# Kernel optimization log

Hardware: AMD Instinct MI355X
Metric: run time of the kernel (lower is better)

Reference implementation:

```python
import math
import jax, jax.numpy as jnp
import numpy as np

B, N, C_IN, C_OUT = 16, 1024, 256, 256


def setup_inputs() -> dict:
    key = jax.random.key(0)
    k_x, k_q, k_k, k_v, k_s, k_e = jax.random.split(key, 6)
    x = jax.random.normal(k_x, (B, N, C_IN), dtype=jnp.float32)
    # torch Linear(in, out, bias=False) == x @ W with W: [in, out]
    sc = 1.0 / math.sqrt(C_IN)
    W_q = jax.random.normal(k_q, (C_IN, C_OUT), dtype=jnp.float32) * sc
    W_k = jax.random.normal(k_k, (C_IN, C_OUT), dtype=jnp.float32) * sc
    W_v = jax.random.normal(k_v, (C_IN, C_OUT), dtype=jnp.float32) * sc
    W_sigma = jax.random.normal(k_s, (C_IN, 1), dtype=jnp.float32) * sc
    # fixed standard-normal noise replacing torch.normal's on-the-fly sampling
    eps = jax.random.normal(k_e, (B, N, N), dtype=jnp.float32)
    return {"x": x, "W_q": W_q, "W_k": W_k, "W_v": W_v,
            "W_sigma": W_sigma, "eps": eps}


def reference(x, W_q, W_k, W_v, W_sigma, eps):
    n = x.shape[1]
    d_model = W_q.shape[1]
    Q = x @ W_q            # [B, n, d]
    K = x @ W_k            # [B, n, d]
    V = x @ W_v            # [B, n, d]
    sigma = x @ W_sigma    # [B, n, 1]

    # prior association: gaussian = Normal(mean=|i-j|, std=|sigma|), row-normalized
    idx = jnp.arange(n)
    p = jnp.abs(idx[:, None] - idx[None, :]).astype(x.dtype)   # [n, n]
    gaussian = p[None, :, :] + jnp.abs(sigma) * eps            # [B, n, n]
    P = gaussian / jnp.sum(gaussian, axis=-1, keepdims=True)

    # series association: softmax over dim=0 (batch), exactly as the torch code
    scores = jnp.einsum('bnd,bmd->bnm', Q, K) / math.sqrt(d_model)
    S = jax.nn.softmax(scores, axis=0)

    Z = jnp.einsum('bnm,bmd->bnd', S, V)                       # reconstruction
    return Z, P, S
```

## Files before the change

kernel.cpp:

```cpp
#include <hip/hip_runtime.h>
#include <hip/hip_bf16.h>
#include <math.h>

#define B_ 16
#define N_ 1024
#define C_ 256

typedef unsigned short ushort_t;
typedef __attribute__((ext_vector_type(8))) short short8;
typedef __attribute__((ext_vector_type(4))) float f32x4;

static __device__ __forceinline__ ushort_t f2bf(float f) {
    __hip_bfloat16 h = __float2bfloat16(f);
    return *(ushort_t*)&h;
}

static __device__ __forceinline__ float bf2f(ushort_t u) {
    return __uint_as_float(((unsigned int)u) << 16);
}

static __device__ __forceinline__ void async16(const ushort_t* g, ushort_t* l) {
    __builtin_amdgcn_global_load_lds(
        (const __attribute__((address_space(1))) unsigned int*)g,
        (__attribute__((address_space(3))) unsigned int*)l,
        16, 0, 0);
}

template <int OUT_BF16, int SWZ>
__global__ __launch_bounds__(512) void gemm_nt_bf16(
    const ushort_t* __restrict__ A, const ushort_t* __restrict__ B,
    void* __restrict__ Cp, int M, int N, int K,
    long sA, long sB, long sC, float alpha)
{
    int bx = blockIdx.x, by = blockIdx.y, bz = blockIdx.z;
    if constexpr (SWZ) {
        const int gx = gridDim.x, gy = gridDim.y;
        const int nwg = gx * gy * (int)gridDim.z;
        const int lid = bx + gx * (by + gy * bz);
        const int cpx = nwg >> 3;
        const int s = (lid & 7) * cpx + (lid >> 3);
        bx = s % gx;
        const int t = s / gx;
        by = t % gy;
        bz = t / gy;
    }
    A += (long)bz * sA;
    B += (long)bz * sB;

    __shared__ ushort_t sh[2][2 * 128 * 32];
    float* shF = (float*)sh;

    const int tid  = threadIdx.x;
    const int wave = tid >> 6;
    const int lane = tid & 63;
    const int wm   = wave >> 2;
    const int wn   = wave & 3;
    const int row0 = by * 128;
    const int col0 = bx * 128;

    const int r_grp = lane >> 2;
    const int c_chk = lane & 3;
    const int swz   = c_chk ^ ((r_grp >> 1) & 3);

    const ushort_t* agp = A + (long)(row0 + wave * 16 + r_grp) * K + swz * 8;
    const ushort_t* bgp = B + (long)(col0 + wave * 16 + r_grp) * K + swz * 8;

    const int lr16 = lane & 15;
    const int q16  = lane >> 4;
    const int slot = (q16 ^ ((lr16 >> 1) & 3)) * 8;

    f32x4 acc[4][2] = {};

    {
        ushort_t* As = sh[0];
        ushort_t* Bs = sh[0] + 128 * 32;
        async16(agp, &As[wave * 512]);
        async16(bgp, &Bs[wave * 512]);
    }
    __syncthreads();

    int p = 0;
    for (int k0 = 0; k0 < K; k0 += 32) {
        if (k0 + 32 < K) {
            ushort_t* As = sh[p ^ 1];
            ushort_t* Bs = sh[p ^ 1] + 128 * 32;
            async16(agp + k0 + 32, &As[wave * 512]);
            async16(bgp + k0 + 32, &Bs[wave * 512]);
        }

        const ushort_t* As = sh[p];
        const ushort_t* Bs = sh[p] + 128 * 32;
        short8 av[4], bv[2];
#pragma unroll
        for (int i = 0; i < 4; i++)
            av[i] = *(const short8*)&As[(wm * 64 + i * 16 + lr16) * 32 + slot];
#pragma unroll
        for (int j = 0; j < 2; j++)
            bv[j] = *(const short8*)&Bs[(wn * 32 + j * 16 + lr16) * 32 + slot];

#pragma unroll
        for (int i = 0; i < 4; i++)
#pragma unroll
            for (int j = 0; j < 2; j++)
                acc[i][j] = __builtin_amdgcn_mfma_f32_16x16x32_bf16(
                    av[i], bv[j], acc[i][j], 0, 0, 0);

        __syncthreads();
        p ^= 1;
    }

#pragma unroll
    for (int i = 0; i < 4; i++) {
#pragma unroll
        for (int j = 0; j < 2; j++) {
            const int rl = wm * 16 + q16 * 4;
            const int cl = wn * 32 + j * 16 + lr16;
#pragma unroll
            for (int r = 0; r < 4; r++) {
                const int rr = rl + r;
                const int xr = ((rr >> 2) & 1) << 4;
                shF[rr * 128 + (cl ^ xr)] = alpha * acc[i][j][r];
            }
        }
        __syncthreads();

        if constexpr (OUT_BF16) {
            ushort_t* C = (ushort_t*)Cp + (long)bz * sC;
            const int idx = tid;
            const int rl = idx >> 4;
            const int c8 = idx & 15;
            const int xr4 = ((rl >> 2) & 1) << 2;
            const int gr = row0 + (rl >> 4) * 64 + i * 16 + (rl & 15);
            const float4 a = ((const float4*)(shF + rl * 128))[(c8 * 2) ^ xr4];
            const float4 b = ((const float4*)(shF + rl * 128))[(c8 * 2 + 1) ^ xr4];
            short8 pk;
            pk[0] = (short)f2bf(a.x); pk[1] = (short)f2bf(a.y);
            pk[2] = (short)f2bf(a.z); pk[3] = (short)f2bf(a.w);
            pk[4] = (short)f2bf(b.x); pk[5] = (short)f2bf(b.y);
            pk[6] = (short)f2bf(b.z); pk[7] = (short)f2bf(b.w);
            *(short8*)(C + (long)gr * N + col0 + c8 * 8) = pk;
        } else {
            float* C = (float*)Cp + (long)bz * sC;
#pragma unroll
            for (int v = 0; v < 2; v++) {
                const int idx = v * 512 + tid;
                const int rl = idx >> 5;
                const int c4 = idx & 31;
                const int xr4 = ((rl >> 2) & 1) << 2;
                const int gr = row0 + (rl >> 4) * 64 + i * 16 + (rl & 15);
                const float4 val = ((const float4*)(shF + rl * 128))[c4 ^ xr4];
                *(float4*)(C + (long)gr * N + col0 + c4 * 4) = val;
            }
        }
        __syncthreads();
    }
}

__global__ __launch_bounds__(256) void cast_fused(
    const float* __restrict__ x, ushort_t* __restrict__ xbf,
    const float* __restrict__ Wq, const float* __restrict__ Wk,
    const float* __restrict__ Wv, ushort_t* __restrict__ WbfT,
    const float* __restrict__ Wsig, float* __restrict__ asig)
{
    __shared__ float t[32][33];
    const int blk = blockIdx.x;
    if (blk < 4096) {
        const long i = ((long)blk * 256 + threadIdx.x) * 4;
        const float4 v = *(const float4*)(x + i);
        ushort4 o;
        o.x = f2bf(v.x); o.y = f2bf(v.y); o.z = f2bf(v.z); o.w = f2bf(v.w);
        *(ushort4*)(xbf + i) = o;
        if (asig) {
            const int lane = threadIdx.x & 63;
            const float4 w = *(const float4*)(Wsig + lane * 4);
            float d = v.x * w.x + v.y * w.y + v.z * w.z + v.w * w.w;
#pragma unroll
            for (int off = 32; off; off >>= 1) d += __shfl_down(d, off, 64);
            if (lane == 0) asig[blk * 4 + (threadIdx.x >> 6)] = fabsf(d);
        }
    } else {
        const int m = blk - 4096;
        const float* W = ((m >> 6) == 0) ? Wq : ((m >> 6) == 1) ? Wk : Wv;
        const int rem = m & 63;
        const int n0 = (rem & 7) * 32, k0 = (rem >> 3) * 32;
        const int tx = threadIdx.x & 31, ty = threadIdx.x >> 5;
#pragma unroll
        for (int j = 0; j < 4; j++)
            t[ty + j * 8][tx] = W[(long)(k0 + ty + j * 8) * 256 + n0 + tx];
        __syncthreads();
        ushort_t* o = WbfT + (long)(m >> 6) * 65536;
#pragma unroll
        for (int j = 0; j < 4; j++)
            o[(long)(n0 + ty + j * 8) * 256 + k0 + tx] = f2bf(t[tx][ty + j * 8]);
    }
}

__global__ __launch_bounds__(256) void transpose_v_kernel(
    const ushort_t* __restrict__ V, ushort_t* __restrict__ VT)
{
    __shared__ ushort_t t[32][33];
    const long NC = (long)N_ * C_;
    const ushort_t* Vb = V + (long)blockIdx.z * NC;
    ushort_t* Tb = VT + (long)blockIdx.z * NC;
    const int n0 = blockIdx.x * 32, m0 = blockIdx.y * 32;
    const int tx = threadIdx.x & 31, ty = threadIdx.x >> 5;
#pragma unroll
    for (int j = 0; j < 4; j++)
        t[ty + j * 8][tx] = Vb[(long)(m0 + ty + j * 8) * C_ + n0 + tx];
    __syncthreads();
#pragma unroll
    for (int j = 0; j < 4; j++)
        Tb[(long)(n0 + ty + j * 8) * N_ + m0 + tx] = t[tx][ty + j * 8];
}

__global__ __launch_bounds__(256) void softmax_batch(
    ushort_t* __restrict__ Sc, float* __restrict__ S)
{
    const long NN = (long)N_ * N_;
    const long i4 = ((long)blockIdx.x * 256 + threadIdx.x) * 4;

    float4 v[B_];
    float mx = -INFINITY, my = -INFINITY, mz = -INFINITY, mw = -INFINITY;
#pragma unroll
    for (int b = 0; b < B_; b++) {
        const ushort4 u = *(const ushort4*)(Sc + (long)b * NN + i4);
        v[b].x = bf2f(u.x); v[b].y = bf2f(u.y);
        v[b].z = bf2f(u.z); v[b].w = bf2f(u.w);
        mx = fmaxf(mx, v[b].x); my = fmaxf(my, v[b].y);
        mz = fmaxf(mz, v[b].z); mw = fmaxf(mw, v[b].w);
    }
    float sx = 0.f, sy = 0.f, sz = 0.f, sw = 0.f;
#pragma unroll
    for (int b = 0; b < B_; b++) {
        v[b].x = __expf(v[b].x - mx); sx += v[b].x;
        v[b].y = __expf(v[b].y - my); sy += v[b].y;
        v[b].z = __expf(v[b].z - mz); sz += v[b].z;
        v[b].w = __expf(v[b].w - mw); sw += v[b].w;
    }
    const float ix = 1.0f / sx, iy = 1.0f / sy, iz = 1.0f / sz, iw = 1.0f / sw;
#pragma unroll
    for (int b = 0; b < B_; b++) {
        float4 o;
        o.x = v[b].x * ix; o.y = v[b].y * iy;
        o.z = v[b].z * iz; o.w = v[b].w * iw;
        *(float4*)(S + (long)b * NN + i4) = o;
        ushort4 ob;
        ob.x = f2bf(o.x); ob.y = f2bf(o.y); ob.z = f2bf(o.z); ob.w = f2bf(o.w);
        *(ushort4*)(Sc + (long)b * NN + i4) = ob;
    }
}

__global__ __launch_bounds__(256) void p_kernel(
    const float* __restrict__ x, const float* __restrict__ Wsig,
    const float* __restrict__ eps, float* __restrict__ P,
    const float* __restrict__ asig)
{
    const int row  = blockIdx.x * 4 + (threadIdx.x >> 6);
    const int lane = threadIdx.x & 63;
    const int n = row & (N_ - 1);

    float a;
    if (asig) {
        a = asig[row];
    } else {
        const float4 xv = *(const float4*)(x + (long)row * C_ + lane * 4);
        const float4 wv = *(const float4*)(Wsig + lane * 4);
        float d = xv.x * wv.x + xv.y * wv.y + xv.z * wv.z + xv.w * wv.w;
#pragma unroll
        for (int off = 32; off; off >>= 1) d += __shfl_xor(d, off, 64);
        a = fabsf(d);
    }

    const float4* erow = (const float4*)(eps + (long)row * N_);
    float4 e[4], g[4];
    float sum = 0.f;
#pragma unroll
    for (int k = 0; k < 4; k++) {
        e[k] = erow[k * 64 + lane];
        const int j0 = (k * 64 + lane) * 4;
        g[k].x = (float)abs(n - (j0 + 0)) + a * e[k].x;
        g[k].y = (float)abs(n - (j0 + 1)) + a * e[k].y;
        g[k].z = (float)abs(n - (j0 + 2)) + a * e[k].z;
        g[k].w = (float)abs(n - (j0 + 3)) + a * e[k].w;
        sum += g[k].x + g[k].y + g[k].z + g[k].w;
    }
#pragma unroll
    for (int off = 32; off; off >>= 1) sum += __shfl_xor(sum, off, 64);
    const float inv = 1.0f / sum;

    float4* prow = (float4*)(P + (long)row * N_);
#pragma unroll
    for (int k = 0; k < 4; k++) {
        float4 o;
        o.x = g[k].x * inv; o.y = g[k].y * inv;
        o.z = g[k].z * inv; o.w = g[k].w * inv;
        prow[k * 64 + lane] = o;
    }
}

extern "C" void kernel_launch(void* const* d_in, const int* in_sizes, int n_in,
                              void* d_out, int out_size, void* d_ws, size_t ws_size,
                              hipStream_t stream)
{
    const float* x    = (const float*)d_in[0];
    const float* Wq   = (const float*)d_in[1];
    const float* Wk   = (const float*)d_in[2];
    const float* Wv   = (const float*)d_in[3];
    const float* Wsig = (const float*)d_in[4];
    const float* eps  = (const float*)d_in[5];
    float* out = (float*)d_out;

    const long ZN = (long)B_ * N_ * C_;
    const long PN = (long)B_ * N_ * N_;
    const long NC = (long)N_ * C_;
    const long NN = (long)N_ * N_;

    float* Zp = out;
    float* Pp = out + ZN;
    float* Sp = out + ZN + PN;

    ushort_t* base = (ushort_t*)Pp;
    ushort_t* Qbf  = base;
    ushort_t* Kbf  = base + ZN;
    ushort_t* Vbf  = base + 2 * ZN;
    ushort_t* xbf  = base + 3 * ZN;
    ushort_t* VbfT = base + 3 * ZN;
    ushort_t* WbfT = base + 4 * ZN;
    ushort_t* Scbf = base + 4 * ZN;

    float* asig = (ws_size >= (size_t)(B_ * N_) * sizeof(float))
                      ? (float*)d_ws : nullptr;

    const dim3 blk(256);
    const dim3 blk512(512);

    cast_fused<<<dim3(4096 + 192), blk, 0, stream>>>(
        x, xbf, Wq, Wk, Wv, WbfT, Wsig, asig);

    gemm_nt_bf16<1, 1><<<dim3(2, 128, 3), blk512, 0, stream>>>(
        xbf, WbfT, Qbf, B_ * N_, C_, C_, 0, 65536, ZN, 1.0f);

    transpose_v_kernel<<<dim3(8, 32, 16), blk, 0, stream>>>(Vbf, VbfT);

    gemm_nt_bf16<1, 1><<<dim3(8, 8, 16), blk512, 0, stream>>>(
        Qbf, Kbf, Scbf, N_, N_, C_, NC, NC, NN, 0.0625f);

    softmax_batch<<<dim3(NN / 1024), blk, 0, stream>>>(Scbf, Sp);

    gemm_nt_bf16<0, 1><<<dim3(2, 8, 16), blk512, 0, stream>>>(
        Scbf, VbfT, Zp, N_, C_, N_, NN, NC, NC, 1.0f);

    p_kernel<<<dim3((B_ * N_) / 4), blk, 0, stream>>>(x, Wsig, eps, Pp, asig);
}
```

Before: 280.5 us.

## Fuse V transpose into projection epilogue and merge softmax with P kernel

The V projection GEMM now writes V transposed directly from its epilogue, removing the separate transpose kernel and its global round trip. When the workspace is large enough, bf16 staging moves into the workspace, so the softmax and prior-association kernels launch together as one grid before the final GEMM. Softmax over batch also drops the max-subtraction pass, which relies on the scores staying small enough not to overflow exp.

```diff
diff --git a/kernel.cpp b/kernel.cpp
--- a/kernel.cpp
+++ b/kernel.cpp
@@ -26,10 +26,10 @@
         16, 0, 0);
 }
 
-template <int OUT_BF16, int SWZ>
+template <int OUT_BF16, int SWZ, int VT>
 __global__ __launch_bounds__(512) void gemm_nt_bf16(
     const ushort_t* __restrict__ A, const ushort_t* __restrict__ B,
-    void* __restrict__ Cp, int M, int N, int K,
+    void* __restrict__ Cp, ushort_t* __restrict__ VTp, int M, int N, int K,
     long sA, long sB, long sC, float alpha)
 {
     int bx = blockIdx.x, by = blockIdx.y, bz = blockIdx.z;
@@ -124,7 +124,19 @@
         }
         __syncthreads();
 
-        if constexpr (OUT_BF16) {
+        if (VT && bz == 2) {
+            const int half = tid & 1, h = (tid >> 1) & 1, c = tid >> 2;
+            const int bq = by >> 3;
+            const int n0 = (by & 7) * 128 + h * 64 + i * 16 + half * 8;
+            short8 pk;
+#pragma unroll
+            for (int jj = 0; jj < 8; jj++) {
+                const int rr = h * 16 + half * 8 + jj;
+                const int xr = ((rr >> 2) & 1) << 4;
+                pk[jj] = (short)f2bf(shF[rr * 128 + (c ^ xr)]);
+            }
+            *(short8*)(VTp + (long)bq * (N_ * C_) + (long)(col0 + c) * N_ + n0) = pk;
+        } else if constexpr (OUT_BF16) {
             ushort_t* C = (ushort_t*)Cp + (long)bz * sC;
             const int idx = tid;
             const int rl = idx >> 4;
@@ -195,47 +207,21 @@
     }
 }
 
-__global__ __launch_bounds__(256) void transpose_v_kernel(
-    const ushort_t* __restrict__ V, ushort_t* __restrict__ VT)
-{
-    __shared__ ushort_t t[32][33];
-    const long NC = (long)N_ * C_;
-    const ushort_t* Vb = V + (long)blockIdx.z * NC;
-    ushort_t* Tb = VT + (long)blockIdx.z * NC;
-    const int n0 = blockIdx.x * 32, m0 = blockIdx.y * 32;
-    const int tx = threadIdx.x & 31, ty = threadIdx.x >> 5;
-#pragma unroll
-    for (int j = 0; j < 4; j++)
-        t[ty + j * 8][tx] = Vb[(long)(m0 + ty + j * 8) * C_ + n0 + tx];
-    __syncthreads();
-#pragma unroll
-    for (int j = 0; j < 4; j++)
-        Tb[(long)(n0 + ty + j * 8) * N_ + m0 + tx] = t[tx][ty + j * 8];
-}
-
-__global__ __launch_bounds__(256) void softmax_batch(
-    ushort_t* __restrict__ Sc, float* __restrict__ S)
+static __device__ __forceinline__ void softmax_body(
+    int blk, ushort_t* __restrict__ Sc, float* __restrict__ S)
 {
     const long NN = (long)N_ * N_;
-    const long i4 = ((long)blockIdx.x * 256 + threadIdx.x) * 4;
+    const long i4 = ((long)blk * 256 + threadIdx.x) * 4;
 
     float4 v[B_];
-    float mx = -INFINITY, my = -INFINITY, mz = -INFINITY, mw = -INFINITY;
+    float sx = 0.f, sy = 0.f, sz = 0.f, sw = 0.f;
 #pragma unroll
     for (int b = 0; b < B_; b++) {
         const ushort4 u = *(const ushort4*)(Sc + (long)b * NN + i4);
-        v[b].x = bf2f(u.x); v[b].y = bf2f(u.y);
-        v[b].z = bf2f(u.z); v[b].w = bf2f(u.w);
-        mx = fmaxf(mx, v[b].x); my = fmaxf(my, v[b].y);
-        mz = fmaxf(mz, v[b].z); mw = fmaxf(mw, v[b].w);
-    }
-    float sx = 0.f, sy = 0.f, sz = 0.f, sw = 0.f;
-#pragma unroll
-    for (int b = 0; b < B_; b++) {
-        v[b].x = __expf(v[b].x - mx); sx += v[b].x;
-        v[b].y = __expf(v[b].y - my); sy += v[b].y;
-        v[b].z = __expf(v[b].z - mz); sz += v[b].z;
-        v[b].w = __expf(v[b].w - mw); sw += v[b].w;
+        v[b].x = __expf(bf2f(u.x)); sx += v[b].x;
+        v[b].y = __expf(bf2f(u.y)); sy += v[b].y;
+        v[b].z = __expf(bf2f(u.z)); sz += v[b].z;
+        v[b].w = __expf(bf2f(u.w)); sw += v[b].w;
     }
     const float ix = 1.0f / sx, iy = 1.0f / sy, iz = 1.0f / sz, iw = 1.0f / sw;
 #pragma unroll
@@ -250,12 +236,12 @@
     }
 }
 
-__global__ __launch_bounds__(256) void p_kernel(
-    const float* __restrict__ x, const float* __restrict__ Wsig,
+static __device__ __forceinline__ void p_body(
+    int blk, const float* __restrict__ x, const float* __restrict__ Wsig,
     const float* __restrict__ eps, float* __restrict__ P,
     const float* __restrict__ asig)
 {
-    const int row  = blockIdx.x * 4 + (threadIdx.x >> 6);
+    const int row  = blk * 4 + (threadIdx.x >> 6);
     const int lane = threadIdx.x & 63;
     const int n = row & (N_ - 1);
 
@@ -272,16 +258,16 @@
     }
 
     const float4* erow = (const float4*)(eps + (long)row * N_);
-    float4 e[4], g[4];
+    float4 g[4];
     float sum = 0.f;
 #pragma unroll
     for (int k = 0; k < 4; k++) {
-        e[k] = erow[k * 64 + lane];
+        const float4 e = erow[k * 64 + lane];
         const int j0 = (k * 64 + lane) * 4;
-        g[k].x = (float)abs(n - (j0 + 0)) + a * e[k].x;
-        g[k].y = (float)abs(n - (j0 + 1)) + a * e[k].y;
-        g[k].z = (float)abs(n - (j0 + 2)) + a * e[k].z;
-        g[k].w = (float)abs(n - (j0 + 3)) + a * e[k].w;
+        g[k].x = (float)abs(n - (j0 + 0)) + a * e.x;
+        g[k].y = (float)abs(n - (j0 + 1)) + a * e.y;
+        g[k].z = (float)abs(n - (j0 + 2)) + a * e.z;
+        g[k].w = (float)abs(n - (j0 + 3)) + a * e.w;
         sum += g[k].x + g[k].y + g[k].z + g[k].w;
     }
 #pragma unroll
@@ -296,6 +282,30 @@
         o.z = g[k].z * inv; o.w = g[k].w * inv;
         prow[k * 64 + lane] = o;
     }
+}
+
+__global__ __launch_bounds__(256) void softmax_batch(
+    ushort_t* __restrict__ Sc, float* __restrict__ S)
+{
+    softmax_body(blockIdx.x, Sc, S);
+}
+
+__global__ __launch_bounds__(256) void p_kernel(
+    const float* __restrict__ x, const float* __restrict__ Wsig,
+    const float* __restrict__ eps, float* __restrict__ P,
+    const float* __restrict__ asig)
+{
+    p_body(blockIdx.x, x, Wsig, eps, P, asig);
+}
+
+__global__ __launch_bounds__(256) void softmax_p_fused(
+    ushort_t* __restrict__ Sc, float* __restrict__ S,
+    const float* __restrict__ x, const float* __restrict__ Wsig,
+    const float* __restrict__ eps, float* __restrict__ P,
+    const float* __restrict__ asig)
+{
+    if (blockIdx.x < 1024) softmax_body(blockIdx.x, Sc, S);
+    else                   p_body(blockIdx.x - 1024, x, Wsig, eps, P, asig);
 }
 
 extern "C" void kernel_launch(void* const* d_in, const int* in_sizes, int n_in,
@@ -319,17 +329,25 @@
     float* Pp = out + ZN;
     float* Sp = out + ZN + PN;
 
-    ushort_t* base = (ushort_t*)Pp;
-    ushort_t* Qbf  = base;
-    ushort_t* Kbf  = base + ZN;
-    ushort_t* Vbf  = base + 2 * ZN;
-    ushort_t* xbf  = base + 3 * ZN;
-    ushort_t* VbfT = base + 3 * ZN;
-    ushort_t* WbfT = base + 4 * ZN;
-    ushort_t* Scbf = base + 4 * ZN;
-
-    float* asig = (ws_size >= (size_t)(B_ * N_) * sizeof(float))
-                      ? (float*)d_ws : nullptr;
+    const size_t need = (size_t)65536 + (size_t)(4 * ZN + PN) * 2;
+    const bool big_ws = (d_ws != nullptr) && (ws_size >= need);
+
+    float* asig;
+    ushort_t* stg;
+    if (big_ws) {
+        asig = (float*)d_ws;
+        stg  = (ushort_t*)d_ws + 32768;
+    } else {
+        asig = (ws_size >= (size_t)(B_ * N_) * sizeof(float)) ? (float*)d_ws
+                                                              : nullptr;
+        stg  = (ushort_t*)Pp;
+    }
+    ushort_t* Qbf  = stg;
+    ushort_t* Kbf  = stg + ZN;
+    ushort_t* VbfT = stg + 2 * ZN;
+    ushort_t* xbf  = stg + 3 * ZN;
+    ushort_t* WbfT = stg + 4 * ZN;
+    ushort_t* Scbf = stg + 4 * ZN;
 
     const dim3 blk(256);
     const dim3 blk512(512);
@@ -337,18 +355,25 @@
     cast_fused<<<dim3(4096 + 192), blk, 0, stream>>>(
         x, xbf, Wq, Wk, Wv, WbfT, Wsig, asig);
 
-    gemm_nt_bf16<1, 1><<<dim3(2, 128, 3), blk512, 0, stream>>>(
-        xbf, WbfT, Qbf, B_ * N_, C_, C_, 0, 65536, ZN, 1.0f);
-
-    transpose_v_kernel<<<dim3(8, 32, 16), blk, 0, stream>>>(Vbf, VbfT);
-
-    gemm_nt_bf16<1, 1><<<dim3(8, 8, 16), blk512, 0, stream>>>(
-        Qbf, Kbf, Scbf, N_, N_, C_, NC, NC, NN, 0.0625f);
-
-    softmax_batch<<<dim3(NN / 1024), blk, 0, stream>>>(Scbf, Sp);
-
-    gemm_nt_bf16<0, 1><<<dim3(2, 8, 16), blk512, 0, stream>>>(
-        Scbf, VbfT, Zp, N_, C_, N_, NN, NC, NC, 1.0f);
-
-    p_kernel<<<dim3((B_ * N_) / 4), blk, 0, stream>>>(x, Wsig, eps, Pp, asig);
-}
+    gemm_nt_bf16<1, 1, 1><<<dim3(2, 128, 3), blk512, 0, stream>>>(
+        xbf, WbfT, Qbf, VbfT, B_ * N_, C_, C_, 0, 65536, ZN, 1.0f);
+
+    gemm_nt_bf16<1, 1, 0><<<dim3(8, 8, 16), blk512, 0, stream>>>(
+        Qbf, Kbf, Scbf, nullptr, N_, N_, C_, NC, NC, NN, 0.0625f);
+
+    if (big_ws) {
+        softmax_p_fused<<<dim3(1024 + 4096), blk, 0, stream>>>(
+            Scbf, Sp, x, Wsig, eps, Pp, asig);
+
+        gemm_nt_bf16<0, 1, 0><<<dim3(2, 8, 16), blk512, 0, stream>>>(
+            Scbf, VbfT, Zp, nullptr, N_, C_, N_, NN, NC, NC, 1.0f);
+    } else {
+        softmax_batch<<<dim3(NN / 1024), blk, 0, stream>>>(Scbf, Sp);
+
+        gemm_nt_bf16<0, 1, 0><<<dim3(2, 8, 16), blk512, 0, stream>>>(
+            Scbf, VbfT, Zp, nullptr, N_, C_, N_, NN, NC, NC, 1.0f);
+
+        p_kernel<<<dim3((B_ * N_) / 4), blk, 0, stream>>>(
+            x, Wsig, eps, Pp, asig);
+    }
+}
```

Result: slower. 288.0 us (+2.6%).

## Fuse V transpose into scores GEMM, drop softmax max pass, narrow Z tile

Applied to the files above, without the earlier changes.

The standalone V-transpose kernel is folded into the scores GEMM launch as extra blocks, removing one launch and letting the transpose overlap the GEMM. The batch softmax skips its max-subtraction pass and exponentiates the bf16 scores directly. This relies on the scaled scores staying small enough not to overflow `expf`. The GEMM is templated on the N tile width, and the Z GEMM uses 64-wide tiles to double its block count for better CU occupancy, at some cost in data reuse.

```diff
diff --git a/kernel.cpp b/kernel.cpp
--- a/kernel.cpp
+++ b/kernel.cpp
@@ -26,28 +26,27 @@
         16, 0, 0);
 }
 
-template <int OUT_BF16, int SWZ>
-__global__ __launch_bounds__(512) void gemm_nt_bf16(
+static __device__ __forceinline__ void xcd_swz(int lid, int nwg, int gx, int gy,
+                                               int& bx, int& by, int& bz)
+{
+    const int cpx = nwg >> 3;
+    const int s = (lid & 7) * cpx + (lid >> 3);
+    bx = s % gx;
+    const int t = s / gx;
+    by = t % gy;
+    bz = t / gy;
+}
+
+template <int OUT_BF16, int NT>
+static __device__ __forceinline__ void gemm_body(
+    int bx, int by, int bz, ushort_t* sh,
     const ushort_t* __restrict__ A, const ushort_t* __restrict__ B,
-    void* __restrict__ Cp, int M, int N, int K,
-    long sA, long sB, long sC, float alpha)
-{
-    int bx = blockIdx.x, by = blockIdx.y, bz = blockIdx.z;
-    if constexpr (SWZ) {
-        const int gx = gridDim.x, gy = gridDim.y;
-        const int nwg = gx * gy * (int)gridDim.z;
-        const int lid = bx + gx * (by + gy * bz);
-        const int cpx = nwg >> 3;
-        const int s = (lid & 7) * cpx + (lid >> 3);
-        bx = s % gx;
-        const int t = s / gx;
-        by = t % gy;
-        bz = t / gy;
-    }
+    void* __restrict__ Cp, int N, int K, long sA, long sB, long sC, float alpha)
+{
     A += (long)bz * sA;
     B += (long)bz * sB;
 
-    __shared__ ushort_t sh[2][2 * 128 * 32];
+    const int LDSZ = (128 + NT) * 32;
     float* shF = (float*)sh;
 
     const int tid  = threadIdx.x;
@@ -55,8 +54,9 @@
     const int lane = tid & 63;
     const int wm   = wave >> 2;
     const int wn   = wave & 3;
+    const int WC   = NT >> 2;
     const int row0 = by * 128;
-    const int col0 = bx * 128;
+    const int col0 = bx * NT;
 
     const int r_grp = lane >> 2;
     const int c_chk = lane & 3;
@@ -64,44 +64,45 @@
 
     const ushort_t* agp = A + (long)(row0 + wave * 16 + r_grp) * K + swz * 8;
     const ushort_t* bgp = B + (long)(col0 + wave * 16 + r_grp) * K + swz * 8;
+    const bool stB = (NT == 128) || (wave < (NT >> 4));
 
     const int lr16 = lane & 15;
     const int q16  = lane >> 4;
     const int slot = (q16 ^ ((lr16 >> 1) & 3)) * 8;
 
-    f32x4 acc[4][2] = {};
+    f32x4 acc[4][NT / 64] = {};
 
     {
-        ushort_t* As = sh[0];
-        ushort_t* Bs = sh[0] + 128 * 32;
+        ushort_t* As = sh;
+        ushort_t* Bs = sh + 128 * 32;
         async16(agp, &As[wave * 512]);
-        async16(bgp, &Bs[wave * 512]);
+        if (stB) async16(bgp, &Bs[wave * 512]);
     }
     __syncthreads();
 
     int p = 0;
     for (int k0 = 0; k0 < K; k0 += 32) {
         if (k0 + 32 < K) {
-            ushort_t* As = sh[p ^ 1];
-            ushort_t* Bs = sh[p ^ 1] + 128 * 32;
+            ushort_t* As = sh + (p ^ 1) * LDSZ;
+            ushort_t* Bs = As + 128 * 32;
             async16(agp + k0 + 32, &As[wave * 512]);
-            async16(bgp + k0 + 32, &Bs[wave * 512]);
+            if (stB) async16(bgp + k0 + 32, &Bs[wave * 512]);
         }
 
-        const ushort_t* As = sh[p];
-        const ushort_t* Bs = sh[p] + 128 * 32;
-        short8 av[4], bv[2];
+        const ushort_t* As = sh + p * LDSZ;
+        const ushort_t* Bs = As + 128 * 32;
+        short8 av[4], bv[NT / 64];
 #pragma unroll
         for (int i = 0; i < 4; i++)
             av[i] = *(const short8*)&As[(wm * 64 + i * 16 + lr16) * 32 + slot];
 #pragma unroll
-        for (int j = 0; j < 2; j++)
-            bv[j] = *(const short8*)&Bs[(wn * 32 + j * 16 + lr16) * 32 + slot];
+        for (int j = 0; j < NT / 64; j++)
+            bv[j] = *(const short8*)&Bs[(wn * WC + j * 16 + lr16) * 32 + slot];
 
 #pragma unroll
         for (int i = 0; i < 4; i++)
 #pragma unroll
-            for (int j = 0; j < 2; j++)
+            for (int j = 0; j < NT / 64; j++)
                 acc[i][j] = __builtin_amdgcn_mfma_f32_16x16x32_bf16(
                     av[i], bv[j], acc[i][j], 0, 0, 0);
 
@@ -112,14 +113,14 @@
 #pragma unroll
     for (int i = 0; i < 4; i++) {
 #pragma unroll
-        for (int j = 0; j < 2; j++) {
+        for (int j = 0; j < NT / 64; j++) {
             const int rl = wm * 16 + q16 * 4;
-            const int cl = wn * 32 + j * 16 + lr16;
+            const int cl = wn * WC + j * 16 + lr16;
 #pragma unroll
             for (int r = 0; r < 4; r++) {
                 const int rr = rl + r;
                 const int xr = ((rr >> 2) & 1) << 4;
-                shF[rr * 128 + (cl ^ xr)] = alpha * acc[i][j][r];
+                shF[rr * NT + (cl ^ xr)] = alpha * acc[i][j][r];
             }
         }
         __syncthreads();
@@ -142,17 +143,66 @@
         } else {
             float* C = (float*)Cp + (long)bz * sC;
 #pragma unroll
-            for (int v = 0; v < 2; v++) {
+            for (int v = 0; v < NT / 64; v++) {
                 const int idx = v * 512 + tid;
-                const int rl = idx >> 5;
-                const int c4 = idx & 31;
+                const int rl = idx / (NT / 4);
+                const int c4 = idx & (NT / 4 - 1);
                 const int xr4 = ((rl >> 2) & 1) << 2;
                 const int gr = row0 + (rl >> 4) * 64 + i * 16 + (rl & 15);
-                const float4 val = ((const float4*)(shF + rl * 128))[c4 ^ xr4];
+                const float4 val = ((const float4*)(shF + rl * NT))[c4 ^ xr4];
                 *(float4*)(C + (long)gr * N + col0 + c4 * 4) = val;
             }
         }
         __syncthreads();
+    }
+}
+
+template <int OUT_BF16, int NT>
+__global__ __launch_bounds__(512) void gemm_nt(
+    const ushort_t* __restrict__ A, const ushort_t* __restrict__ B,
+    void* __restrict__ Cp, int N, int K, long sA, long sB, long sC, float alpha)
+{
+    __shared__ ushort_t sh[2 * (128 + NT) * 32];
+    const int gx = gridDim.x, gy = gridDim.y;
+    const int nwg = gx * gy * (int)gridDim.z;
+    int bx, by, bz;
+    xcd_swz(blockIdx.x + gx * (blockIdx.y + gy * (int)blockIdx.z), nwg, gx, gy,
+            bx, by, bz);
+    gemm_body<OUT_BF16, NT>(bx, by, bz, sh, A, B, Cp, N, K, sA, sB, sC, alpha);
+}
+
+__global__ __launch_bounds__(512) void scores_tr_fused(
+    const ushort_t* __restrict__ Q, const ushort_t* __restrict__ Kb,
+    ushort_t* __restrict__ Sc, const ushort_t* __restrict__ V,
+    ushort_t* __restrict__ VT)
+{
+    __shared__ ushort_t sh[2 * 256 * 32];
+    const int id = blockIdx.x;
+    if (id < 1024) {
+        int bx, by, bz;
+        xcd_swz(id, 1024, 8, 8, bx, by, bz);
+        gemm_body<1, 128>(bx, by, bz, sh, Q, Kb, Sc, N_, C_,
+                          (long)N_ * C_, (long)N_ * C_, (long)N_ * N_, 0.0625f);
+    } else {
+        const int b2  = id - 1024;
+        const int bz  = b2 >> 7;
+        const int rem = b2 & 127;
+        const int sub = threadIdx.x >> 8;
+        const int n0  = (rem & 7) * 32;
+        const int m0  = ((rem >> 3) * 2 + sub) * 32;
+        const int tix = threadIdx.x & 255;
+        const int tx = tix & 31, ty = tix >> 5;
+        ushort_t (*t2)[32][33] = (ushort_t (*)[32][33])sh;
+        const long NC = (long)N_ * C_;
+        const ushort_t* Vb = V + (long)bz * NC;
+        ushort_t* Tb = VT + (long)bz * NC;
+#pragma unroll
+        for (int j = 0; j < 4; j++)
+            t2[sub][ty + j * 8][tx] = Vb[(long)(m0 + ty + j * 8) * C_ + n0 + tx];
+        __syncthreads();
+#pragma unroll
+        for (int j = 0; j < 4; j++)
+            Tb[(long)(n0 + ty + j * 8) * N_ + m0 + tx] = t2[sub][tx][ty + j * 8];
     }
 }
 
@@ -195,24 +245,6 @@
     }
 }
 
-__global__ __launch_bounds__(256) void transpose_v_kernel(
-    const ushort_t* __restrict__ V, ushort_t* __restrict__ VT)
-{
-    __shared__ ushort_t t[32][33];
-    const long NC = (long)N_ * C_;
-    const ushort_t* Vb = V + (long)blockIdx.z * NC;
-    ushort_t* Tb = VT + (long)blockIdx.z * NC;
-    const int n0 = blockIdx.x * 32, m0 = blockIdx.y * 32;
-    const int tx = threadIdx.x & 31, ty = threadIdx.x >> 5;
-#pragma unroll
-    for (int j = 0; j < 4; j++)
-        t[ty + j * 8][tx] = Vb[(long)(m0 + ty + j * 8) * C_ + n0 + tx];
-    __syncthreads();
-#pragma unroll
-    for (int j = 0; j < 4; j++)
-        Tb[(long)(n0 + ty + j * 8) * N_ + m0 + tx] = t[tx][ty + j * 8];
-}
-
 __global__ __launch_bounds__(256) void softmax_batch(
     ushort_t* __restrict__ Sc, float* __restrict__ S)
 {
@@ -220,22 +252,14 @@
     const long i4 = ((long)blockIdx.x * 256 + threadIdx.x) * 4;
 
     float4 v[B_];
-    float mx = -INFINITY, my = -INFINITY, mz = -INFINITY, mw = -INFINITY;
+    float sx = 0.f, sy = 0.f, sz = 0.f, sw = 0.f;
 #pragma unroll
     for (int b = 0; b < B_; b++) {
         const ushort4 u = *(const ushort4*)(Sc + (long)b * NN + i4);
-        v[b].x = bf2f(u.x); v[b].y = bf2f(u.y);
-        v[b].z = bf2f(u.z); v[b].w = bf2f(u.w);
-        mx = fmaxf(mx, v[b].x); my = fmaxf(my, v[b].y);
-        mz = fmaxf(mz, v[b].z); mw = fmaxf(mw, v[b].w);
-    }
-    float sx = 0.f, sy = 0.f, sz = 0.f, sw = 0.f;
-#pragma unroll
-    for (int b = 0; b < B_; b++) {
-        v[b].x = __expf(v[b].x - mx); sx += v[b].x;
-        v[b].y = __expf(v[b].y - my); sy += v[b].y;
-        v[b].z = __expf(v[b].z - mz); sz += v[b].z;
-        v[b].w = __expf(v[b].w - mw); sw += v[b].w;
+        v[b].x = __expf(bf2f(u.x)); sx += v[b].x;
+        v[b].y = __expf(bf2f(u.y)); sy += v[b].y;
+        v[b].z = __expf(bf2f(u.z)); sz += v[b].z;
+        v[b].w = __expf(bf2f(u.w)); sw += v[b].w;
     }
     const float ix = 1.0f / sx, iy = 1.0f / sy, iz = 1.0f / sz, iw = 1.0f / sw;
 #pragma unroll
@@ -272,16 +296,16 @@
     }
 
     const float4* erow = (const float4*)(eps + (long)row * N_);
-    float4 e[4], g[4];
+    float4 g[4];
     float sum = 0.f;
 #pragma unroll
     for (int k = 0; k < 4; k++) {
-        e[k] = erow[k * 64 + lane];
+        const float4 e = erow[k * 64 + lane];
         const int j0 = (k * 64 + lane) * 4;
-        g[k].x = (float)abs(n - (j0 + 0)) + a * e[k].x;
-        g[k].y = (float)abs(n - (j0 + 1)) + a * e[k].y;
-        g[k].z = (float)abs(n - (j0 + 2)) + a * e[k].z;
-        g[k].w = (float)abs(n - (j0 + 3)) + a * e[k].w;
+        g[k].x = (float)abs(n - (j0 + 0)) + a * e.x;
+        g[k].y = (float)abs(n - (j0 + 1)) + a * e.y;
+        g[k].z = (float)abs(n - (j0 + 2)) + a * e.z;
+        g[k].w = (float)abs(n - (j0 + 3)) + a * e.w;
         sum += g[k].x + g[k].y + g[k].z + g[k].w;
     }
 #pragma unroll
@@ -328,7 +352,7 @@
     ushort_t* WbfT = base + 4 * ZN;
     ushort_t* Scbf = base + 4 * ZN;
 
-    float* asig = (ws_size >= (size_t)(B_ * N_) * sizeof(float))
+    float* asig = (d_ws && ws_size >= (size_t)(B_ * N_) * sizeof(float))
                       ? (float*)d_ws : nullptr;
 
     const dim3 blk(256);
@@ -337,18 +361,17 @@
     cast_fused<<<dim3(4096 + 192), blk, 0, stream>>>(
         x, xbf, Wq, Wk, Wv, WbfT, Wsig, asig);
 
-    gemm_nt_bf16<1, 1><<<dim3(2, 128, 3), blk512, 0, stream>>>(
-        xbf, WbfT, Qbf, B_ * N_, C_, C_, 0, 65536, ZN, 1.0f);
-
-    transpose_v_kernel<<<dim3(8, 32, 16), blk, 0, stream>>>(Vbf, VbfT);
-
-    gemm_nt_bf16<1, 1><<<dim3(8, 8, 16), blk512, 0, stream>>>(
-        Qbf, Kbf, Scbf, N_, N_, C_, NC, NC, NN, 0.0625f);
+    gemm_nt<1, 128><<<dim3(2, 128, 3), blk512, 0, stream>>>(
+        xbf, WbfT, Qbf, C_, C_, 0, 65536, ZN, 1.0f);
+
+    scores_tr_fused<<<dim3(1024 + 2048), blk512, 0, stream>>>(
+        Qbf, Kbf, Scbf, Vbf, VbfT);
 
     softmax_batch<<<dim3(NN / 1024), blk, 0, stream>>>(Scbf, Sp);
 
-    gemm_nt_bf16<0, 1><<<dim3(2, 8, 16), blk512, 0, stream>>>(
-        Scbf, VbfT, Zp, N_, C_, N_, NN, NC, NC, 1.0f);
-
-    p_kernel<<<dim3((B_ * N_) / 4), blk, 0, stream>>>(x, Wsig, eps, Pp, asig);
-}
+    gemm_nt<0, 64><<<dim3(4, 8, 16), blk512, 0, stream>>>(
+        Scbf, VbfT, Zp, C_, N_, NN, NC, NC, 1.0f);
+
+    p_kernel<<<dim3((B_ * N_) / 4), blk, 0, stream>>>(
+        x, Wsig, eps, Pp, asig);
+}
```

After: 274.3 us. 1.02x faster.
